# Kernel optimization log

Measured on AMD Instinct MI355X. Metric: run time of the kernel, lower is better.

Reference implementation:

```python
import jax, jax.numpy as jnp
import numpy as np

BS, D, M = 64, 256, 512


def setup_inputs() -> dict:
    key = jax.random.key(0)
    ks = jax.random.split(key, 6)
    # Small scales keep the 10-step RLS recurrence numerically stable.
    A_start = 0.05 * jax.random.normal(ks[0], (BS, D, D), dtype=jnp.float32)
    Y1 = 0.05 * jax.random.normal(ks[1], (BS, D, M), dtype=jnp.float32)
    Y2 = 0.05 * jax.random.normal(ks[2], (BS, D, M), dtype=jnp.float32)
    y1 = 0.05 * jax.random.normal(ks[3], (BS, D, 1), dtype=jnp.float32)
    y2 = 0.05 * jax.random.normal(ks[4], (BS, D, 1), dtype=jnp.float32)
    eye = jnp.broadcast_to(jnp.eye(D, dtype=jnp.float32), (BS, D, D))
    P_inv_start = 1e-3 * eye + 1e-4 * jax.random.normal(ks[5], (BS, D, D), dtype=jnp.float32)
    return {"A_start": A_start, "Y1": Y1, "Y2": Y2, "y1": y1, "y2": y2,
            "P_inv_start": P_inv_start, "h": 2, "m_prox": 10}


def _t(x):
    return jnp.swapaxes(x, 1, 2)


def reference(A_start, Y1, Y2, y1, y2, P_inv_start, h, m_prox):
    """Faithful jax version of DelayedDMD.update.

    The torch code recomputes `A_t + P_inv @ (Y1 @ (Y2^T - Y1^T @ A_t))` twice
    per step; here it is computed once (same math, fused).
    """
    Y1t, Y2t, y1t, y2t = _t(Y1), _t(Y2), _t(y1), _t(y2)
    denom = 1.0 + y1t @ P_inv_start @ y1          # (bs, 1, 1)
    Piy1 = P_inv_start @ y1                       # (bs, d, 1)

    def step(A_t, _):
        # batch recursive-least-squares prox iteration
        M_ = A_t + P_inv_start @ (Y1 @ (Y2t - Y1t @ A_t))   # (bs, d, d)
        A_new = M_ + y1 @ (y2t - y1t @ M_) / denom
        return A_new, None

    A_final_t, _ = jax.lax.scan(step, _t(A_start), None, length=m_prox)
    P_inv_new = P_inv_start - Piy1 @ (y1t @ P_inv_start) / denom
    return _t(A_final_t), P_inv_new
```

## Files before the change

kernel.cpp:

```cpp
#include <hip/hip_runtime.h>
#include <hip/hip_bf16.h>
#include <stdint.h>


#define BSZ 64
#define DD 256
#define MM 512

typedef __attribute__((ext_vector_type(8))) short short8;
typedef __attribute__((ext_vector_type(4))) float f32x4;

__device__ __forceinline__ unsigned short f2b(float f) {
    unsigned int u = __float_as_uint(f);
    unsigned int r = (u + 0x7fffu + ((u >> 16) & 1u)) >> 16;
    return (unsigned short)r;
}
__device__ __forceinline__ float b2f(unsigned short s) {
    return __uint_as_float(((unsigned int)s) << 16);
}

#define GLDS16(gp, lp)                                                                   \
    __builtin_amdgcn_global_load_lds((const __attribute__((address_space(1))) void*)(gp),\
                                     (__attribute__((address_space(3))) void*)(lp),      \
                                     16, 0, 0)

__global__ __launch_bounds__(256)
void veck1(const float* __restrict__ P, const float* __restrict__ y1, float* __restrict__ vec)
{
    const int b = blockIdx.y, c0 = blockIdx.x * 64;
    const float* Pb = P + (long)b * DD * DD;
    float* vb = vec + (long)b * 2048;
    const int t = threadIdx.x, wv = t >> 6, ln = t & 63;
    __shared__ float sy1[DD];
    __shared__ float red[256];
    sy1[t] = y1[b * DD + t];
    __syncthreads();
    for (int rr = 0; rr < 16; ++rr) {
        const int r = c0 + wv * 16 + rr;
        float s = 0.f;
#pragma unroll
        for (int cc = 0; cc < 4; ++cc) s += Pb[(long)r * DD + cc * 64 + ln] * sy1[cc * 64 + ln];
        for (int o = 32; o; o >>= 1) s += __shfl_down(s, o, 64);
        if (ln == 0) vb[r] = s;
    }
    {
        const int j = c0 + (t & 63);
        const int l0 = (t >> 6) * 64;
        float s = 0.f;
        for (int l = l0; l < l0 + 64; ++l) s += sy1[l] * Pb[(long)l * DD + j];
        red[t] = s;
        __syncthreads();
        if (t < 64) vb[256 + c0 + t] = red[t] + red[64 + t] + red[128 + t] + red[192 + t];
    }
}

__global__ __launch_bounds__(256)
void veck3(const float* __restrict__ y1, float* __restrict__ vec)
{
    const int b = blockIdx.x, t = threadIdx.x;
    float* vb = vec + (long)b * 2048;
    __shared__ float red[256];
    red[t] = vb[t] * y1[b * DD + t];
    __syncthreads();
    for (int s = 128; s; s >>= 1) { if (t < s) red[t] += red[t + s]; __syncthreads(); }
    if (t == 0) vb[1024] = 1.0f / (1.0f + red[0]);
}

__global__ __launch_bounds__(256)
void convP(const float* __restrict__ P, const float* __restrict__ vec,
           unsigned short* __restrict__ Pb, float* __restrict__ out2)
{
    const int b = blockIdx.y;
    const long base = (long)b * DD * DD;
    const float* vb = vec + (long)b * 2048;
    const int idx = (blockIdx.x * 256 + threadIdx.x) * 4;
    const int i = idx >> 8, j = idx & 255;
    const float kPi = vb[1024] * vb[i];
    float4 p = *(const float4*)(P + base + idx);
    ushort4 o;
    o.x = f2b(p.x); o.y = f2b(p.y); o.z = f2b(p.z); o.w = f2b(p.w);
    *(ushort4*)(Pb + base + idx) = o;
    float4 q = *(const float4*)(vb + 256 + j);
    float4 r;
    r.x = p.x - kPi * q.x; r.y = p.y - kPi * q.y;
    r.z = p.z - kPi * q.z; r.w = p.w - kPi * q.w;
    *(float4*)(out2 + base + idx) = r;
}

__global__ __launch_bounds__(256)
void convY(const float* __restrict__ Y1, const float* __restrict__ Y2,
           unsigned short* __restrict__ D1, unsigned short* __restrict__ D2)
{
    const long H = (long)BSZ * DD * MM;
    long i4 = ((long)blockIdx.x * 256 + threadIdx.x) * 4;
    const float* s; unsigned short* d; long off;
    if (i4 < H) { s = Y1; d = D1; off = i4; } else { s = Y2; d = D2; off = i4 - H; }
    float4 v = *(const float4*)(s + off);
    ushort4 o;
    o.x = f2b(v.x); o.y = f2b(v.y); o.z = f2b(v.z); o.w = f2b(v.w);
    *(ushort4*)(d + off) = o;
}

template<int KD, int EPI>
__global__ __launch_bounds__(256)
void gemmk(const unsigned short* __restrict__ A1, const unsigned short* __restrict__ B1,
           unsigned short* __restrict__ O1,
           const unsigned short* __restrict__ A2, const unsigned short* __restrict__ B2,
           unsigned short* __restrict__ O2,
           const float* __restrict__ vec, const float* __restrict__ y1g)
{
    __shared__ __align__(16) unsigned short As[128 * 32];
    __shared__ __align__(16) unsigned short Bs[128 * 32];
    const int z = blockIdx.z, sel = z >> 6, b = z & 63;
    const int i0 = blockIdx.y * 128, j0 = blockIdx.x * 128;
    const unsigned short* Ab = (sel ? A2 : A1) + (long)b * DD * KD;
    const unsigned short* Bb = (sel ? B2 : B1) + (long)b * DD * KD;
    unsigned short* Ob = (sel ? O2 : O1) + (long)b * DD * DD;
    const int t = threadIdx.x, wv = t >> 6, ln = t & 63;
    const int lr = ln & 15, qd = ln >> 4;
    const int mh = (wv >> 1) * 64, nh = (wv & 1) * 64;

    const int g0 = wv * 64 + ln;
    const int g1 = 256 + wv * 64 + ln;
    const int r0g = g0 >> 2, k0g = (g0 & 3) * 8;
    const int r1g = g1 >> 2, k1g = (g1 & 3) * 8;

    f32x4 acc[4][4] = {};

    for (int kc = 0; kc < KD; kc += 32) {
        GLDS16(Ab + (long)(i0 + r0g) * KD + kc + k0g, As + g0 * 8);
        GLDS16(Ab + (long)(i0 + r1g) * KD + kc + k1g, As + g1 * 8);
        GLDS16(Bb + (long)(j0 + r0g) * KD + kc + k0g, Bs + g0 * 8);
        GLDS16(Bb + (long)(j0 + r1g) * KD + kc + k1g, Bs + g1 * 8);
        __syncthreads();
        short8 af[4], bfr[4];
#pragma unroll
        for (int mt = 0; mt < 4; ++mt)
            af[mt] = *(const short8*)(As + (mh + mt * 16 + lr) * 32 + qd * 8);
#pragma unroll
        for (int nt = 0; nt < 4; ++nt)
            bfr[nt] = *(const short8*)(Bs + (nh + nt * 16 + lr) * 32 + qd * 8);
#pragma unroll
        for (int mt = 0; mt < 4; ++mt)
#pragma unroll
            for (int nt = 0; nt < 4; ++nt)
                acc[mt][nt] = __builtin_amdgcn_mfma_f32_16x16x32_bf16(
                    af[mt], bfr[nt], acc[mt][nt], 0, 0, 0);
        __syncthreads();
    }

    const float* vb = vec ? (vec + (long)b * 2048) : nullptr;
    const float* rvp = (EPI == 1) ? (vb + (sel ? 1536 : 1280)) : nullptr;
    const float* cvp = (EPI == 1) ? (sel ? (y1g + (long)b * DD) : (vb + 512)) : nullptr;
    const float sg = sel ? 1.f : -1.f;

#pragma unroll
    for (int mt = 0; mt < 4; ++mt) {
#pragma unroll
        for (int nt = 0; nt < 4; ++nt) {
            const int gr0 = i0 + mh + mt * 16 + qd * 4;
            const int gc  = j0 + nh + nt * 16 + lr;
            float cv = 0.f, rv[4];
            if (EPI == 1) {
                cv = cvp[gc];
#pragma unroll
                for (int r = 0; r < 4; ++r) rv[r] = rvp[gr0 + r];
            }
#pragma unroll
            for (int r = 0; r < 4; ++r) {
                const long off = (long)(gr0 + r) * DD + gc;
                if (EPI == 0) Ob[off] = f2b(acc[mt][nt][r]);
                else          Ob[off] = f2b(sg * (acc[mt][nt][r] + rv[r] * cv));
            }
        }
    }
}

__global__ __launch_bounds__(256)
void veckWU(const unsigned short* __restrict__ G1b, const unsigned short* __restrict__ G21b,
            const float* __restrict__ y1, const float* __restrict__ y2,
            float* __restrict__ vec)
{
    const int b = blockIdx.y, c0 = blockIdx.x * 64;
    const unsigned short* G1_ = G1b + (long)b * DD * DD;
    const unsigned short* G2_ = G21b + (long)b * DD * DD;
    float* vb = vec + (long)b * 2048;
    const int t = threadIdx.x, wv = t >> 6, ln = t & 63;
    __shared__ float sq[DD];
    sq[t] = vb[256 + t];
    __syncthreads();
    const float k = vb[1024];
    for (int rr = 0; rr < 16; ++rr) {
        const int r = c0 + wv * 16 + rr;
        float s1 = 0.f, s2 = 0.f;
#pragma unroll
        for (int cc = 0; cc < 4; ++cc) {
            const float qv = sq[cc * 64 + ln];
            s1 += b2f(G1_[(long)r * DD + cc * 64 + ln]) * qv;
            s2 += b2f(G2_[(long)r * DD + cc * 64 + ln]) * qv;
        }
        for (int o = 32; o; o >>= 1) {
            s1 += __shfl_down(s1, o, 64);
            s2 += __shfl_down(s2, o, 64);
        }
        if (ln == 0) {
            const float y1r = y1[b * DD + r];
            vb[512 + r]  = y1r - s1;
            vb[768 + r]  = s2;
            vb[1280 + r] = k * y1r;
            vb[1536 + r] = k * (y2[b * DD + r] - s2);
        }
    }
}

#define ASTRIDE 264
__global__ __launch_bounds__(256, 1)
void iterk(const float* __restrict__ A_start, const unsigned short* __restrict__ Enb,
           const unsigned short* __restrict__ Vpb, float* __restrict__ out1)
{
    __shared__ __align__(16) unsigned short Ash[64 * ASTRIDE];
    const int b = blockIdx.y, r0 = blockIdx.x * 64;
    const long base = (long)b * DD * DD;
    const float* Ab = A_start + base;
    const unsigned short* Eb = Enb + base;
    const unsigned short* Vb = Vpb + base;
    float* Ob = out1 + base;
    const int t = threadIdx.x, wv = t >> 6, ln = t & 63;
    const int lr = ln & 15, qd = ln >> 4;

    f32x4 acc[4][4], vv[4][4];
    short8 ef[4][8];

#pragma unroll
    for (int mt = 0; mt < 4; ++mt)
#pragma unroll
        for (int j = 0; j < 4; ++j) {
            const int col = (wv * 4 + j) * 16 + lr;
            const int rowb = r0 + mt * 16 + qd * 4;
#pragma unroll
            for (int r = 0; r < 4; ++r) {
                const long o = (long)(rowb + r) * DD + col;
                acc[mt][j][r] = Ab[o];
                vv[mt][j][r]  = b2f(Vb[o]);
            }
        }
#pragma unroll
    for (int j = 0; j < 4; ++j) {
        const int n = (wv * 4 + j) * 16 + lr;
#pragma unroll
        for (int kc = 0; kc < 8; ++kc)
            ef[j][kc] = *(const short8*)(Eb + (long)n * DD + kc * 32 + qd * 8);
    }

#pragma unroll 1
    for (int s = 0; s < 10; ++s) {
#pragma unroll
        for (int mt = 0; mt < 4; ++mt)
#pragma unroll
            for (int j = 0; j < 4; ++j) {
                const int col = (wv * 4 + j) * 16 + lr;
#pragma unroll
                for (int r = 0; r < 4; ++r)
                    Ash[(mt * 16 + qd * 4 + r) * ASTRIDE + col] = f2b(acc[mt][j][r]);
            }
#pragma unroll
        for (int mt = 0; mt < 4; ++mt)
#pragma unroll
            for (int j = 0; j < 4; ++j)
                acc[mt][j] += vv[mt][j];
        __syncthreads();
#pragma unroll
        for (int kc = 0; kc < 8; ++kc) {
            short8 af[4];
#pragma unroll
            for (int mt = 0; mt < 4; ++mt)
                af[mt] = *(const short8*)(Ash + (mt * 16 + lr) * ASTRIDE + kc * 32 + qd * 8);
#pragma unroll
            for (int mt = 0; mt < 4; ++mt)
#pragma unroll
                for (int j = 0; j < 4; ++j)
                    acc[mt][j] = __builtin_amdgcn_mfma_f32_16x16x32_bf16(
                        af[mt], ef[j][kc], acc[mt][j], 0, 0, 0);
        }
        __syncthreads();
    }

#pragma unroll
    for (int mt = 0; mt < 4; ++mt)
#pragma unroll
        for (int j = 0; j < 4; ++j) {
            const int col = (wv * 4 + j) * 16 + lr;
            const int rowb = r0 + mt * 16 + qd * 4;
#pragma unroll
            for (int r = 0; r < 4; ++r)
                Ob[(long)(rowb + r) * DD + col] = acc[mt][j][r];
        }
}

extern "C" void kernel_launch(void* const* d_in, const int* in_sizes, int n_in,
                              void* d_out, int out_size, void* d_ws, size_t ws_size,
                              hipStream_t stream)
{
    const float* A_start = (const float*)d_in[0];
    const float* Y1      = (const float*)d_in[1];
    const float* Y2      = (const float*)d_in[2];
    const float* y1      = (const float*)d_in[3];
    const float* y2      = (const float*)d_in[4];
    const float* P       = (const float*)d_in[5];

    const long EL2 = (long)BSZ * DD * DD;

    float* out1 = (float*)d_out;
    float* out2 = out1 + EL2;
    unsigned short* Y1b = (unsigned short*)out1;

    char* w8 = (char*)d_ws;
    unsigned short* Pb   = (unsigned short*)(w8);
    unsigned short* G1b  = (unsigned short*)(w8 + 8388608);
    unsigned short* G21b = (unsigned short*)(w8 + 16777216);
    unsigned short* Y2b  = (unsigned short*)(w8 + 25165824);
    unsigned short* Enb  = (unsigned short*)(w8 + 25165824);
    unsigned short* Vpb  = (unsigned short*)(w8 + 33554432);
    float*          vec  = (float*)(w8 + 41943040);

    const dim3 blk(256);

    veck1<<<dim3(4, BSZ), blk, 0, stream>>>(P, y1, vec);
    veck3<<<BSZ, blk, 0, stream>>>(y1, vec);
    convP<<<dim3(64, BSZ), blk, 0, stream>>>(P, vec, Pb, out2);
    convY<<<16384, blk, 0, stream>>>(Y1, Y2, Y1b, Y2b);

    gemmk<MM, 0><<<dim3(2, 2, 128), blk, 0, stream>>>(Y1b, Y1b, G1b, Y2b, Y1b, G21b,
                                                      nullptr, nullptr);
    veckWU<<<dim3(4, BSZ), blk, 0, stream>>>(G1b, G21b, y1, y2, vec);

    gemmk<DD, 1><<<dim3(2, 2, 128), blk, 0, stream>>>(Pb, G1b, Enb, G21b, Pb, Vpb,
                                                      vec, y1);

    iterk<<<dim3(4, BSZ), blk, 0, stream>>>(A_start, Enb, Vpb, out1);
}
```

Measured before the change: 243.3 us.

## Merge prep kernels, fold vector products into GEMM, retile iteration kernel

The eight launches become four. The Y conversion and the P·y1 vector work now share one kernel, and the Y Gram GEMM and the P conversion/update share a second. The G·q matvecs, formerly a separate kernel, are computed inside the second GEMM's K-loop from the bf16 fragments already in registers. The iteration kernel now uses 32-row tiles with a 2-blocks-per-CU launch bound and an XOR-swizzled LDS layout in place of padding. Together these cut launch overhead and raise occupancy. The matvecs now run on bf16-rounded G values rather than stored bf16 outputs, and the extra VALU work in the GEMM loop is a cost.

```diff
diff --git a/kernel.cpp b/kernel.cpp
--- a/kernel.cpp
+++ b/kernel.cpp
@@ -24,114 +24,169 @@
                                      (__attribute__((address_space(3))) void*)(lp),      \
                                      16, 0, 0)
 
+
 __global__ __launch_bounds__(256)
-void veck1(const float* __restrict__ P, const float* __restrict__ y1, float* __restrict__ vec)
-{
-    const int b = blockIdx.y, c0 = blockIdx.x * 64;
+void prep1(const float* __restrict__ Y1, const float* __restrict__ Y2,
+           const float* __restrict__ y1, const float* __restrict__ P,
+           unsigned short* __restrict__ Y1b, unsigned short* __restrict__ Y2b,
+           float* __restrict__ vec)
+{
+    const int blk = blockIdx.x, t = threadIdx.x;
+    if (blk < 2048) {
+#pragma unroll
+        for (int i = 0; i < 8; ++i) {
+            const long g4 = (long)blk * 2048 + i * 256 + t;
+            const float* s; unsigned short* d; long off;
+            if (g4 < 2097152) { s = Y1; d = Y1b; off = g4 * 4; }
+            else              { s = Y2; d = Y2b; off = (g4 - 2097152) * 4; }
+            float4 v = *(const float4*)(s + off);
+            ushort4 o;
+            o.x = f2b(v.x); o.y = f2b(v.y); o.z = f2b(v.z); o.w = f2b(v.w);
+            *(ushort4*)(d + off) = o;
+        }
+        return;
+    }
+    const int c = blk - 2048, b = c >> 1;
     const float* Pb = P + (long)b * DD * DD;
-    float* vb = vec + (long)b * 2048;
-    const int t = threadIdx.x, wv = t >> 6, ln = t & 63;
+    float* vb = vec + (long)b * 768;
     __shared__ float sy1[DD];
-    __shared__ float red[256];
+    __shared__ float red[DD];
+    __shared__ float pi[DD];
     sy1[t] = y1[b * DD + t];
     __syncthreads();
-    for (int rr = 0; rr < 16; ++rr) {
-        const int r = c0 + wv * 16 + rr;
+    if (c & 1) {
         float s = 0.f;
-#pragma unroll
-        for (int cc = 0; cc < 4; ++cc) s += Pb[(long)r * DD + cc * 64 + ln] * sy1[cc * 64 + ln];
-        for (int o = 32; o; o >>= 1) s += __shfl_down(s, o, 64);
-        if (ln == 0) vb[r] = s;
-    }
-    {
-        const int j = c0 + (t & 63);
-        const int l0 = (t >> 6) * 64;
-        float s = 0.f;
-        for (int l = l0; l < l0 + 64; ++l) s += sy1[l] * Pb[(long)l * DD + j];
-        red[t] = s;
-        __syncthreads();
-        if (t < 64) vb[256 + c0 + t] = red[t] + red[64 + t] + red[128 + t] + red[192 + t];
+        for (int l = 0; l < DD; ++l) s += sy1[l] * Pb[(long)l * DD + t];
+        vb[256 + t] = s;
+    } else {
+        const int wv = t >> 6, ln = t & 63;
+        for (int rr = 0; rr < 64; ++rr) {
+            const int r = wv * 64 + rr;
+            float s = 0.f;
+#pragma unroll
+            for (int cc = 0; cc < 4; ++cc) s += Pb[(long)r * DD + cc * 64 + ln] * sy1[cc * 64 + ln];
+            for (int o = 32; o; o >>= 1) s += __shfl_down(s, o, 64);
+            if (ln == 0) { vb[r] = s; pi[r] = s; }
+        }
+        __syncthreads();
+        red[t] = sy1[t] * pi[t];
+        __syncthreads();
+        for (int s2 = 128; s2; s2 >>= 1) { if (t < s2) red[t] += red[t + s2]; __syncthreads(); }
+        if (t == 0) vb[512] = 1.0f / (1.0f + red[0]);
     }
 }
 
 __global__ __launch_bounds__(256)
-void veck3(const float* __restrict__ y1, float* __restrict__ vec)
-{
-    const int b = blockIdx.x, t = threadIdx.x;
-    float* vb = vec + (long)b * 2048;
-    __shared__ float red[256];
-    red[t] = vb[t] * y1[b * DD + t];
-    __syncthreads();
-    for (int s = 128; s; s >>= 1) { if (t < s) red[t] += red[t + s]; __syncthreads(); }
-    if (t == 0) vb[1024] = 1.0f / (1.0f + red[0]);
-}
-
-__global__ __launch_bounds__(256)
-void convP(const float* __restrict__ P, const float* __restrict__ vec,
+void prep2(const unsigned short* __restrict__ Y1b, const unsigned short* __restrict__ Y2b,
+           const float* __restrict__ P, const float* __restrict__ vec,
+           unsigned short* __restrict__ G1b, unsigned short* __restrict__ G21b,
            unsigned short* __restrict__ Pb, float* __restrict__ out2)
-{
-    const int b = blockIdx.y;
-    const long base = (long)b * DD * DD;
-    const float* vb = vec + (long)b * 2048;
-    const int idx = (blockIdx.x * 256 + threadIdx.x) * 4;
-    const int i = idx >> 8, j = idx & 255;
-    const float kPi = vb[1024] * vb[i];
-    float4 p = *(const float4*)(P + base + idx);
-    ushort4 o;
-    o.x = f2b(p.x); o.y = f2b(p.y); o.z = f2b(p.z); o.w = f2b(p.w);
-    *(ushort4*)(Pb + base + idx) = o;
-    float4 q = *(const float4*)(vb + 256 + j);
-    float4 r;
-    r.x = p.x - kPi * q.x; r.y = p.y - kPi * q.y;
-    r.z = p.z - kPi * q.z; r.w = p.w - kPi * q.w;
-    *(float4*)(out2 + base + idx) = r;
-}
-
-__global__ __launch_bounds__(256)
-void convY(const float* __restrict__ Y1, const float* __restrict__ Y2,
-           unsigned short* __restrict__ D1, unsigned short* __restrict__ D2)
-{
-    const long H = (long)BSZ * DD * MM;
-    long i4 = ((long)blockIdx.x * 256 + threadIdx.x) * 4;
-    const float* s; unsigned short* d; long off;
-    if (i4 < H) { s = Y1; d = D1; off = i4; } else { s = Y2; d = D2; off = i4 - H; }
-    float4 v = *(const float4*)(s + off);
-    ushort4 o;
-    o.x = f2b(v.x); o.y = f2b(v.y); o.z = f2b(v.z); o.w = f2b(v.w);
-    *(ushort4*)(d + off) = o;
-}
-
-template<int KD, int EPI>
-__global__ __launch_bounds__(256)
-void gemmk(const unsigned short* __restrict__ A1, const unsigned short* __restrict__ B1,
-           unsigned short* __restrict__ O1,
-           const unsigned short* __restrict__ A2, const unsigned short* __restrict__ B2,
-           unsigned short* __restrict__ O2,
-           const float* __restrict__ vec, const float* __restrict__ y1g)
 {
     __shared__ __align__(16) unsigned short As[128 * 32];
     __shared__ __align__(16) unsigned short Bs[128 * 32];
+    const int blk = blockIdx.x, t = threadIdx.x;
+    if (blk < 512) {
+        const int quad = blk & 3, z = blk >> 2, sel = z >> 6, b = z & 63;
+        const int i0 = (quad >> 1) * 128, j0 = (quad & 1) * 128;
+        const unsigned short* Ab = (sel ? Y2b : Y1b) + (long)b * DD * MM;
+        const unsigned short* Bb = Y1b + (long)b * DD * MM;
+        unsigned short* Ob = (sel ? G21b : G1b) + (long)b * DD * DD;
+        const int wv = t >> 6, ln = t & 63;
+        const int lr = ln & 15, qd = ln >> 4;
+        const int mh = (wv >> 1) * 64, nh = (wv & 1) * 64;
+        const int g0 = wv * 64 + ln, g1 = 256 + wv * 64 + ln;
+        const int r0g = g0 >> 2, k0g = (g0 & 3) * 8;
+        const int r1g = g1 >> 2, k1g = (g1 & 3) * 8;
+        f32x4 acc[4][4] = {};
+        for (int kc = 0; kc < MM; kc += 32) {
+            GLDS16(Ab + (long)(i0 + r0g) * MM + kc + k0g, As + g0 * 8);
+            GLDS16(Ab + (long)(i0 + r1g) * MM + kc + k1g, As + g1 * 8);
+            GLDS16(Bb + (long)(j0 + r0g) * MM + kc + k0g, Bs + g0 * 8);
+            GLDS16(Bb + (long)(j0 + r1g) * MM + kc + k1g, Bs + g1 * 8);
+            __syncthreads();
+            short8 af[4], bfr[4];
+#pragma unroll
+            for (int mt = 0; mt < 4; ++mt)
+                af[mt] = *(const short8*)(As + (mh + mt * 16 + lr) * 32 + qd * 8);
+#pragma unroll
+            for (int nt = 0; nt < 4; ++nt)
+                bfr[nt] = *(const short8*)(Bs + (nh + nt * 16 + lr) * 32 + qd * 8);
+#pragma unroll
+            for (int mt = 0; mt < 4; ++mt)
+#pragma unroll
+                for (int nt = 0; nt < 4; ++nt)
+                    acc[mt][nt] = __builtin_amdgcn_mfma_f32_16x16x32_bf16(
+                        af[mt], bfr[nt], acc[mt][nt], 0, 0, 0);
+            __syncthreads();
+        }
+#pragma unroll
+        for (int mt = 0; mt < 4; ++mt)
+#pragma unroll
+            for (int nt = 0; nt < 4; ++nt) {
+                const int gr0 = i0 + mh + mt * 16 + qd * 4;
+                const int gc  = j0 + nh + nt * 16 + lr;
+#pragma unroll
+                for (int r = 0; r < 4; ++r)
+                    Ob[(long)(gr0 + r) * DD + gc] = f2b(acc[mt][nt][r]);
+            }
+        return;
+    }
+    const int c = blk - 512, b = c >> 2, rs = (c & 3) * 64;
+    const long base = (long)b * DD * DD;
+    const float* vb = vec + (long)b * 768;
+    const float kk = vb[512];
+#pragma unroll 4
+    for (int i = 0; i < 16; ++i) {
+        const int idx = rs * DD + (i * 256 + t) * 4;
+        const int row = idx >> 8, col = idx & 255;
+        const float kPi = kk * vb[row];
+        float4 p = *(const float4*)(P + base + idx);
+        ushort4 o;
+        o.x = f2b(p.x); o.y = f2b(p.y); o.z = f2b(p.z); o.w = f2b(p.w);
+        *(ushort4*)(Pb + base + idx) = o;
+        float4 q = *(const float4*)(vb + 256 + col);
+        float4 rr;
+        rr.x = p.x - kPi * q.x; rr.y = p.y - kPi * q.y;
+        rr.z = p.z - kPi * q.z; rr.w = p.w - kPi * q.w;
+        *(float4*)(out2 + base + idx) = rr;
+    }
+}
+
+__global__ __launch_bounds__(256)
+void gemmEV(const unsigned short* __restrict__ Pb, const unsigned short* __restrict__ G1b,
+            const unsigned short* __restrict__ G21b,
+            const float* __restrict__ y1g, const float* __restrict__ y2g,
+            const float* __restrict__ vec,
+            unsigned short* __restrict__ Enb, unsigned short* __restrict__ Vpb)
+{
+    __shared__ __align__(16) unsigned short As[128 * 32];
+    __shared__ __align__(16) unsigned short Bs[128 * 32];
+    __shared__ float qs[DD], s1[DD], s2[DD];
     const int z = blockIdx.z, sel = z >> 6, b = z & 63;
     const int i0 = blockIdx.y * 128, j0 = blockIdx.x * 128;
-    const unsigned short* Ab = (sel ? A2 : A1) + (long)b * DD * KD;
-    const unsigned short* Bb = (sel ? B2 : B1) + (long)b * DD * KD;
-    unsigned short* Ob = (sel ? O2 : O1) + (long)b * DD * DD;
+    const unsigned short* Ab = (sel ? G21b : Pb) + (long)b * DD * DD;
+    const unsigned short* Bb = (sel ? Pb : G1b) + (long)b * DD * DD;
+    unsigned short* Ob = (sel ? Vpb : Enb) + (long)b * DD * DD;
+    const float* vb = vec + (long)b * 768;
     const int t = threadIdx.x, wv = t >> 6, ln = t & 63;
     const int lr = ln & 15, qd = ln >> 4;
     const int mh = (wv >> 1) * 64, nh = (wv & 1) * 64;
-
-    const int g0 = wv * 64 + ln;
-    const int g1 = 256 + wv * 64 + ln;
+    const int g0 = wv * 64 + ln, g1 = 256 + wv * 64 + ln;
     const int r0g = g0 >> 2, k0g = (g0 & 3) * 8;
     const int r1g = g1 >> 2, k1g = (g1 & 3) * 8;
 
+    qs[t] = vb[256 + t];
+    s1[t] = y1g[b * DD + t];
+    s2[t] = y2g[b * DD + t];
+
     f32x4 acc[4][4] = {};
-
-    for (int kc = 0; kc < KD; kc += 32) {
-        GLDS16(Ab + (long)(i0 + r0g) * KD + kc + k0g, As + g0 * 8);
-        GLDS16(Ab + (long)(i0 + r1g) * KD + kc + k1g, As + g1 * 8);
-        GLDS16(Bb + (long)(j0 + r0g) * KD + kc + k0g, Bs + g0 * 8);
-        GLDS16(Bb + (long)(j0 + r1g) * KD + kc + k1g, Bs + g1 * 8);
+    float dot[4] = {0.f, 0.f, 0.f, 0.f};
+
+    for (int kc = 0; kc < DD; kc += 32) {
+        GLDS16(Ab + (long)(i0 + r0g) * DD + kc + k0g, As + g0 * 8);
+        GLDS16(Ab + (long)(i0 + r1g) * DD + kc + k1g, As + g1 * 8);
+        GLDS16(Bb + (long)(j0 + r0g) * DD + kc + k0g, Bs + g0 * 8);
+        GLDS16(Bb + (long)(j0 + r1g) * DD + kc + k1g, Bs + g1 * 8);
         __syncthreads();
         short8 af[4], bfr[4];
 #pragma unroll
@@ -140,6 +195,22 @@
 #pragma unroll
         for (int nt = 0; nt < 4; ++nt)
             bfr[nt] = *(const short8*)(Bs + (nh + nt * 16 + lr) * 32 + qd * 8);
+        const float4 qa = *(const float4*)(qs + kc + qd * 8);
+        const float4 qb = *(const float4*)(qs + kc + qd * 8 + 4);
+        const float qf[8] = {qa.x, qa.y, qa.z, qa.w, qb.x, qb.y, qb.z, qb.w};
+        if (!sel) {
+#pragma unroll
+            for (int nt = 0; nt < 4; ++nt)
+#pragma unroll
+                for (int j = 0; j < 8; ++j)
+                    dot[nt] += b2f((unsigned short)bfr[nt][j]) * qf[j];
+        } else {
+#pragma unroll
+            for (int mt = 0; mt < 4; ++mt)
+#pragma unroll
+                for (int j = 0; j < 8; ++j)
+                    dot[mt] += b2f((unsigned short)af[mt][j]) * qf[j];
+        }
 #pragma unroll
         for (int mt = 0; mt < 4; ++mt)
 #pragma unroll
@@ -148,78 +219,45 @@
                     af[mt], bfr[nt], acc[mt][nt], 0, 0, 0);
         __syncthreads();
     }
-
-    const float* vb = vec ? (vec + (long)b * 2048) : nullptr;
-    const float* rvp = (EPI == 1) ? (vb + (sel ? 1536 : 1280)) : nullptr;
-    const float* cvp = (EPI == 1) ? (sel ? (y1g + (long)b * DD) : (vb + 512)) : nullptr;
-    const float sg = sel ? 1.f : -1.f;
-
+#pragma unroll
+    for (int i = 0; i < 4; ++i) {
+        dot[i] += __shfl_xor(dot[i], 16, 64);
+        dot[i] += __shfl_xor(dot[i], 32, 64);
+    }
+    const float kk = vb[512];
 #pragma unroll
     for (int mt = 0; mt < 4; ++mt) {
 #pragma unroll
         for (int nt = 0; nt < 4; ++nt) {
             const int gr0 = i0 + mh + mt * 16 + qd * 4;
             const int gc  = j0 + nh + nt * 16 + lr;
-            float cv = 0.f, rv[4];
-            if (EPI == 1) {
-                cv = cvp[gc];
-#pragma unroll
-                for (int r = 0; r < 4; ++r) rv[r] = rvp[gr0 + r];
-            }
-#pragma unroll
-            for (int r = 0; r < 4; ++r) {
-                const long off = (long)(gr0 + r) * DD + gc;
-                if (EPI == 0) Ob[off] = f2b(acc[mt][nt][r]);
-                else          Ob[off] = f2b(sg * (acc[mt][nt][r] + rv[r] * cv));
-            }
-        }
-    }
-}
-
-__global__ __launch_bounds__(256)
-void veckWU(const unsigned short* __restrict__ G1b, const unsigned short* __restrict__ G21b,
-            const float* __restrict__ y1, const float* __restrict__ y2,
-            float* __restrict__ vec)
-{
-    const int b = blockIdx.y, c0 = blockIdx.x * 64;
-    const unsigned short* G1_ = G1b + (long)b * DD * DD;
-    const unsigned short* G2_ = G21b + (long)b * DD * DD;
-    float* vb = vec + (long)b * 2048;
-    const int t = threadIdx.x, wv = t >> 6, ln = t & 63;
-    __shared__ float sq[DD];
-    sq[t] = vb[256 + t];
-    __syncthreads();
-    const float k = vb[1024];
-    for (int rr = 0; rr < 16; ++rr) {
-        const int r = c0 + wv * 16 + rr;
-        float s1 = 0.f, s2 = 0.f;
-#pragma unroll
-        for (int cc = 0; cc < 4; ++cc) {
-            const float qv = sq[cc * 64 + ln];
-            s1 += b2f(G1_[(long)r * DD + cc * 64 + ln]) * qv;
-            s2 += b2f(G2_[(long)r * DD + cc * 64 + ln]) * qv;
-        }
-        for (int o = 32; o; o >>= 1) {
-            s1 += __shfl_down(s1, o, 64);
-            s2 += __shfl_down(s2, o, 64);
-        }
-        if (ln == 0) {
-            const float y1r = y1[b * DD + r];
-            vb[512 + r]  = y1r - s1;
-            vb[768 + r]  = s2;
-            vb[1280 + r] = k * y1r;
-            vb[1536 + r] = k * (y2[b * DD + r] - s2);
-        }
-    }
-}
-
-#define ASTRIDE 264
-__global__ __launch_bounds__(256, 1)
+            if (!sel) {
+                const float cw = s1[gc] - dot[nt];
+#pragma unroll
+                for (int r = 0; r < 4; ++r) {
+                    const float rv = kk * s1[gr0 + r];
+                    Ob[(long)(gr0 + r) * DD + gc] = f2b(-(acc[mt][nt][r] + rv * cw));
+                }
+            } else {
+                const float cv = s1[gc];
+#pragma unroll
+                for (int r = 0; r < 4; ++r) {
+                    const float uv = __shfl(dot[mt], qd * 4 + r, 64);
+                    const float rv = kk * (s2[gr0 + r] - uv);
+                    Ob[(long)(gr0 + r) * DD + gc] = f2b(acc[mt][nt][r] + rv * cv);
+                }
+            }
+        }
+    }
+}
+
+#define SWZ(row) (((row) ^ ((row) >> 3)) & 7)
+__global__ __launch_bounds__(256, 2)
 void iterk(const float* __restrict__ A_start, const unsigned short* __restrict__ Enb,
            const unsigned short* __restrict__ Vpb, float* __restrict__ out1)
 {
-    __shared__ __align__(16) unsigned short Ash[64 * ASTRIDE];
-    const int b = blockIdx.y, r0 = blockIdx.x * 64;
+    __shared__ __align__(16) unsigned short Ash[32 * 256];
+    const int b = blockIdx.y, r0 = blockIdx.x * 32;
     const long base = (long)b * DD * DD;
     const float* Ab = A_start + base;
     const unsigned short* Eb = Enb + base;
@@ -228,14 +266,14 @@
     const int t = threadIdx.x, wv = t >> 6, ln = t & 63;
     const int lr = ln & 15, qd = ln >> 4;
 
-    f32x4 acc[4][4], vv[4][4];
+    f32x4 acc[2][4], vv[2][4];
     short8 ef[4][8];
 
 #pragma unroll
-    for (int mt = 0; mt < 4; ++mt)
+    for (int mt = 0; mt < 2; ++mt)
 #pragma unroll
         for (int j = 0; j < 4; ++j) {
-            const int col = (wv * 4 + j) * 16 + lr;
+            const int col = wv * 64 + j * 16 + lr;
             const int rowb = r0 + mt * 16 + qd * 4;
 #pragma unroll
             for (int r = 0; r < 4; ++r) {
@@ -246,7 +284,7 @@
         }
 #pragma unroll
     for (int j = 0; j < 4; ++j) {
-        const int n = (wv * 4 + j) * 16 + lr;
+        const int n = wv * 64 + j * 16 + lr;
 #pragma unroll
         for (int kc = 0; kc < 8; ++kc)
             ef[j][kc] = *(const short8*)(Eb + (long)n * DD + kc * 32 + qd * 8);
@@ -254,29 +292,31 @@
 
 #pragma unroll 1
     for (int s = 0; s < 10; ++s) {
-#pragma unroll
-        for (int mt = 0; mt < 4; ++mt)
+        const int cgb = wv * 8 + (lr >> 3), cb = lr & 7;
+#pragma unroll
+        for (int mt = 0; mt < 2; ++mt)
 #pragma unroll
             for (int j = 0; j < 4; ++j) {
-                const int col = (wv * 4 + j) * 16 + lr;
-#pragma unroll
-                for (int r = 0; r < 4; ++r)
-                    Ash[(mt * 16 + qd * 4 + r) * ASTRIDE + col] = f2b(acc[mt][j][r]);
-            }
-#pragma unroll
-        for (int mt = 0; mt < 4; ++mt)
-#pragma unroll
-            for (int j = 0; j < 4; ++j)
+#pragma unroll
+                for (int r = 0; r < 4; ++r) {
+                    const int lrow = mt * 16 + qd * 4 + r;
+                    const int cg = (cgb + j * 2) ^ SWZ(lrow);
+                    Ash[lrow * 256 + cg * 8 + cb] = f2b(acc[mt][j][r]);
+                }
                 acc[mt][j] += vv[mt][j];
+            }
         __syncthreads();
 #pragma unroll
         for (int kc = 0; kc < 8; ++kc) {
-            short8 af[4];
-#pragma unroll
-            for (int mt = 0; mt < 4; ++mt)
-                af[mt] = *(const short8*)(Ash + (mt * 16 + lr) * ASTRIDE + kc * 32 + qd * 8);
-#pragma unroll
-            for (int mt = 0; mt < 4; ++mt)
+            short8 af[2];
+#pragma unroll
+            for (int mt = 0; mt < 2; ++mt) {
+                const int row = mt * 16 + lr;
+                const int cg = (kc * 4 + qd) ^ SWZ(row);
+                af[mt] = *(const short8*)(Ash + row * 256 + cg * 8);
+            }
+#pragma unroll
+            for (int mt = 0; mt < 2; ++mt)
 #pragma unroll
                 for (int j = 0; j < 4; ++j)
                     acc[mt][j] = __builtin_amdgcn_mfma_f32_16x16x32_bf16(
@@ -286,10 +326,10 @@
     }
 
 #pragma unroll
-    for (int mt = 0; mt < 4; ++mt)
+    for (int mt = 0; mt < 2; ++mt)
 #pragma unroll
         for (int j = 0; j < 4; ++j) {
-            const int col = (wv * 4 + j) * 16 + lr;
+            const int col = wv * 64 + j * 16 + lr;
             const int rowb = r0 + mt * 16 + qd * 4;
 #pragma unroll
             for (int r = 0; r < 4; ++r)
@@ -325,17 +365,8 @@
 
     const dim3 blk(256);
 
-    veck1<<<dim3(4, BSZ), blk, 0, stream>>>(P, y1, vec);
-    veck3<<<BSZ, blk, 0, stream>>>(y1, vec);
-    convP<<<dim3(64, BSZ), blk, 0, stream>>>(P, vec, Pb, out2);
-    convY<<<16384, blk, 0, stream>>>(Y1, Y2, Y1b, Y2b);
-
-    gemmk<MM, 0><<<dim3(2, 2, 128), blk, 0, stream>>>(Y1b, Y1b, G1b, Y2b, Y1b, G21b,
-                                                      nullptr, nullptr);
-    veckWU<<<dim3(4, BSZ), blk, 0, stream>>>(G1b, G21b, y1, y2, vec);
-
-    gemmk<DD, 1><<<dim3(2, 2, 128), blk, 0, stream>>>(Pb, G1b, Enb, G21b, Pb, Vpb,
-                                                      vec, y1);
-
-    iterk<<<dim3(4, BSZ), blk, 0, stream>>>(A_start, Enb, Vpb, out1);
-}
+    prep1<<<2176, blk, 0, stream>>>(Y1, Y2, y1, P, Y1b, Y2b, vec);
+    prep2<<<768, blk, 0, stream>>>(Y1b, Y2b, P, vec, G1b, G21b, Pb, out2);
+    gemmEV<<<dim3(2, 2, 128), blk, 0, stream>>>(Pb, G1b, G21b, y1, y2, vec, Enb, Vpb);
+    iterk<<<dim3(8, 64), blk, 0, stream>>>(A_start, Enb, Vpb, out1);
+}
```

After: 245.4 us. Within noise of the previous version (+0.9%).
